# Kernel tuning notes

Measured on AMD Instinct MI355X. Metric: run time of the kernel, lower is better.

The kernel has to match this reference:

```python
import jax, jax.numpy as jnp
import numpy as np

RES_SAMPLE = [-0.4, -0.3, -0.2, -0.1, 0.0, 0.1, 0.2, 0.3, 0.4]
GROUP_NUM = 8


def setup_inputs() -> dict:
    key = jax.random.key(0)
    k1, k2, k3, k4 = jax.random.split(key, 4)
    B, C, H, W = 4, 32, 256, 256
    return {
        "feat_ref": jax.random.normal(k1, (B, C, H, W), dtype=jnp.float32),
        "feat_ls": jax.random.normal(k2, (B, C, H, W), dtype=jnp.float32),
        "feat_rs": jax.random.normal(k3, (B, C, H, W), dtype=jnp.float32),
        "disp_init": jax.random.uniform(k4, (B, 1, H, W), dtype=jnp.float32),
    }


def _bilerp_chw(feat, x, y):
    """Bilinear sample feat [C,H,W] at pixel coords x,y [H,W], zeros padding
    (matches F.grid_sample(mode='bilinear', padding_mode='zeros'))."""
    C, H, W = feat.shape
    x0 = jnp.floor(x); y0 = jnp.floor(y)
    x1 = x0 + 1.0;     y1 = y0 + 1.0
    wx1 = x - x0; wx0 = 1.0 - wx1
    wy1 = y - y0; wy0 = 1.0 - wy1

    def gather(yi, xi):
        valid = (yi >= 0) & (yi <= H - 1) & (xi >= 0) & (xi <= W - 1)
        yc = jnp.clip(yi, 0, H - 1).astype(jnp.int32)
        xc = jnp.clip(xi, 0, W - 1).astype(jnp.int32)
        return feat[:, yc, xc] * valid.astype(feat.dtype)  # [C,H,W]

    return (gather(y0, x0) * (wy0 * wx0)
            + gather(y0, x1) * (wy0 * wx1)
            + gather(y1, x0) * (wy1 * wx0)
            + gather(y1, x1) * (wy1 * wx1))


def _warp_all_disp(feat, disp, x_dist):
    """feat [B,C,H,W], disp [B,D,H,W] -> warped [B,C,D,H,W] (y_dist=0)."""
    B, C, H, W = feat.shape
    xx = jnp.arange(W, dtype=feat.dtype)[None, :] * jnp.ones((H, 1), feat.dtype)  # [H,W]
    yy = jnp.arange(H, dtype=feat.dtype)[:, None] * jnp.ones((1, W), feat.dtype)  # [H,W]

    def per_b(feat_b, disp_b):  # feat_b [C,H,W], disp_b [D,H,W]
        x = xx[None] + x_dist * disp_b                      # [D,H,W]
        y = jnp.broadcast_to(yy, x.shape)                   # [D,H,W]
        return jax.vmap(lambda xs, ys: _bilerp_chw(feat_b, xs, ys))(x, y)  # [D,C,H,W]

    out = jax.vmap(per_b)(feat, disp)                       # [B,D,C,H,W]
    return out.transpose(0, 2, 1, 3, 4)                     # [B,C,D,H,W]


def reference(feat_ref, feat_ls, feat_rs, disp_init):
    B, C, H, W = feat_ref.shape
    res = jnp.asarray(RES_SAMPLE, dtype=feat_ref.dtype)     # [D]
    D = res.shape[0]
    disp = disp_init[:, 0][:, None] + res[None, :, None, None]  # [B,D,H,W]

    warp_left = _warp_all_disp(feat_ls, disp, 1.0)          # [B,C,D,H,W]
    warp_right = _warp_all_disp(feat_rs, disp, -1.0)        # [B,C,D,H,W]
    fr = feat_ref[:, :, None]                                # [B,C,1,H,W]

    mu = (warp_left + warp_right + fr) / 3.0
    var = ((warp_left - mu) ** 2 + (warp_right - mu) ** 2 + (fr - mu) ** 2) / 3.0

    cpg = C // GROUP_NUM
    cost = var.reshape(B, GROUP_NUM, cpg, D, H, W).mean(axis=2)  # [B,G,D,H,W]
    return cost
```

## Files before the change

### kernel.cpp

```cpp
#include <hip/hip_runtime.h>


#define B_ 4
#define C_ 32
#define H_ 256
#define W_ 256
#define D_ 9
#define G_ 8
#define CPG 4
#define HW_ (H_ * W_)

typedef float v2f __attribute__((ext_vector_type(2)));

__global__ __launch_bounds__(256) void cost_volume_kernel(
    const float* __restrict__ fref,
    const float* __restrict__ fls,
    const float* __restrict__ frs,
    const float* __restrict__ disp0,
    float* __restrict__ out)
{
    const float res[D_] = {-0.4f, -0.3f, -0.2f, -0.1f, 0.0f,
                            0.1f,  0.2f,  0.3f,  0.4f};
    int g2 = blockIdx.x & 3;
    int t  = blockIdx.x >> 2;
    int h  = t & (H_ - 1);
    int b  = t >> 8;
    int w  = threadIdx.x;

    float dbase = disp0[((size_t)b * H_ + h) * W_ + w];

    int i0l = (int)floorf((float)w + (dbase + res[0]));
    int i0r = (int)floorf((float)w - (dbase + res[8]));

    float vl[3], vr[3];
    int il[3], ir[3];
    #pragma unroll
    for (int k = 0; k < 3; ++k) {
        int a = i0l + k;
        vl[k] = (a >= 0 && a < W_) ? 1.0f : 0.0f;
        il[k] = min(max(a, 0), W_ - 1);
        int c = i0r + k;
        vr[k] = (c >= 0 && c < W_) ? 1.0f : 0.0f;
        ir[k] = min(max(c, 0), W_ - 1);
    }

    float la[D_], lb[D_], lc[D_];
    float ra[D_], rb[D_], rc[D_];
    #pragma unroll
    for (int d = 0; d < D_; ++d) {
        float disp = dbase + res[d];

        float xl = (float)w + disp;
        float fl = floorf(xl);
        float w1 = xl - fl;
        float w0 = 1.0f - w1;
        bool jl = ((int)fl != i0l);
        la[d] = jl ? 0.0f : w0 * vl[0];
        lb[d] = jl ? w0 * vl[1] : w1 * vl[1];
        lc[d] = jl ? w1 * vl[2] : 0.0f;

        float xr = (float)w - disp;
        float fx = floorf(xr);
        float u1 = xr - fx;
        float u0 = 1.0f - u1;
        bool jr = ((int)fx != i0r);
        ra[d] = jr ? 0.0f : u0 * vr[0];
        rb[d] = jr ? u0 * vr[1] : u1 * vr[1];
        rc[d] = jr ? u1 * vr[2] : 0.0f;
    }

    size_t base = (size_t)b * C_ * HW_ + (size_t)h * W_;
    const float* pref = fref + base;
    const float* pls  = fls  + base;
    const float* prs  = frs  + base;

    size_t obase = (size_t)b * G_ * D_ * HW_ + (size_t)h * W_ + w;

    #pragma unroll 1
    for (int gi = 0; gi < 2; ++gi) {
        int g = g2 * 2 + gi;
        v2f acc[D_];
        #pragma unroll
        for (int d = 0; d < D_; ++d) acc[d] = (v2f)(0.0f);

        #pragma unroll
        for (int p = 0; p < 2; ++p) {
            size_t c0 = (size_t)(g * CPG + p * 2) * HW_;
            const float* rrow = pref + c0;
            const float* lrow = pls + c0;
            const float* rsw  = prs + c0;

            v2f fr = { rrow[w],      rrow[HW_ + w] };
            v2f t0 = { lrow[il[0]],  lrow[HW_ + il[0]] };
            v2f t1 = { lrow[il[1]],  lrow[HW_ + il[1]] };
            v2f t2 = { lrow[il[2]],  lrow[HW_ + il[2]] };
            v2f u0 = { rsw[ir[0]],   rsw[HW_ + ir[0]] };
            v2f u1 = { rsw[ir[1]],   rsw[HW_ + ir[1]] };
            v2f u2 = { rsw[ir[2]],   rsw[HW_ + ir[2]] };

            v2f fr2 = fr * fr;

            #pragma unroll
            for (int d = 0; d < D_; ++d) {
                v2f wl = t0 * la[d] + t1 * lb[d] + t2 * lc[d];
                v2f wr = u0 * ra[d] + u1 * rb[d] + u2 * rc[d];
                v2f s  = wl + wr + fr;
                v2f q  = __builtin_elementwise_fma(
                             wl, wl, __builtin_elementwise_fma(wr, wr, fr2));
                acc[d] += q - s * s * (1.0f / 3.0f);
            }
        }

        #pragma unroll
        for (int d = 0; d < D_; ++d) {
            float v = (acc[d].x + acc[d].y) * (1.0f / 12.0f);
            out[obase + (size_t)(g * D_ + d) * HW_] = v;
        }
    }
}

extern "C" void kernel_launch(void* const* d_in, const int* in_sizes, int n_in,
                              void* d_out, int out_size, void* d_ws, size_t ws_size,
                              hipStream_t stream) {
    const float* fref  = (const float*)d_in[0];
    const float* fls   = (const float*)d_in[1];
    const float* frs   = (const float*)d_in[2];
    const float* disp0 = (const float*)d_in[3];
    float* out = (float*)d_out;

    dim3 grid(B_ * H_ * 4);
    dim3 block(W_);
    cost_volume_kernel<<<grid, block, 0, stream>>>(fref, fls, frs, disp0, out);
}
```

Measured before the change: 170.0 us.

## Stage warped feature rows in LDS via async global_load_lds with zero padding

```diff
diff --git a/kernel.cpp b/kernel.cpp
--- a/kernel.cpp
+++ b/kernel.cpp
@@ -7,12 +7,12 @@
 #define W_ 256
 #define D_ 9
 #define G_ 8
-#define CPG 4
 #define HW_ (H_ * W_)
+#define RSTRIDE 264
 
 typedef float v2f __attribute__((ext_vector_type(2)));
 
-__global__ __launch_bounds__(256) void cost_volume_kernel(
+__global__ __launch_bounds__(256, 4) void cost_volume_kernel(
     const float* __restrict__ fref,
     const float* __restrict__ fls,
     const float* __restrict__ frs,
@@ -21,28 +21,42 @@
 {
     const float res[D_] = {-0.4f, -0.3f, -0.2f, -0.1f, 0.0f,
                             0.1f,  0.2f,  0.3f,  0.4f};
+    __shared__ float smem[16 * RSTRIDE];
+
     int g2 = blockIdx.x & 3;
     int t  = blockIdx.x >> 2;
     int h  = t & (H_ - 1);
     int b  = t >> 8;
     int w  = threadIdx.x;
+    int lane = w & 63;
+    int wave = w >> 6;
+
+    size_t base = (size_t)b * C_ * HW_ + (size_t)h * W_ + (size_t)(g2 * 8) * HW_;
+    const float* pref = fref + base;
+    const float* pls  = fls  + base;
+    const float* prs  = frs  + base;
+
+    #pragma unroll
+    for (int rr = 0; rr < 4; ++rr) {
+        int r  = wave * 4 + rr;
+        int ch = r & 7;
+        const float* grow = ((r < 8) ? pls : prs) + (size_t)ch * HW_ + lane * 4;
+        float* lrow = smem + r * RSTRIDE + 4 + lane * 4;
+        __builtin_amdgcn_global_load_lds(
+            (__attribute__((address_space(1))) unsigned int*)(unsigned long long)grow,
+            (__attribute__((address_space(3))) unsigned int*)lrow,
+            16, 0, 0);
+    }
+    if (w < 128) {
+        int r = w >> 3;
+        int k = w & 7;
+        smem[r * RSTRIDE + ((k < 4) ? k : (256 + k))] = 0.0f;
+    }
 
     float dbase = disp0[((size_t)b * H_ + h) * W_ + w];
 
     int i0l = (int)floorf((float)w + (dbase + res[0]));
     int i0r = (int)floorf((float)w - (dbase + res[8]));
-
-    float vl[3], vr[3];
-    int il[3], ir[3];
-    #pragma unroll
-    for (int k = 0; k < 3; ++k) {
-        int a = i0l + k;
-        vl[k] = (a >= 0 && a < W_) ? 1.0f : 0.0f;
-        il[k] = min(max(a, 0), W_ - 1);
-        int c = i0r + k;
-        vr[k] = (c >= 0 && c < W_) ? 1.0f : 0.0f;
-        ir[k] = min(max(c, 0), W_ - 1);
-    }
 
     float la[D_], lb[D_], lc[D_];
     float ra[D_], rb[D_], rc[D_];
@@ -52,51 +66,55 @@
 
         float xl = (float)w + disp;
         float fl = floorf(xl);
-        float w1 = xl - fl;
-        float w0 = 1.0f - w1;
+        float f1 = xl - fl;
+        float f0 = 1.0f - f1;
         bool jl = ((int)fl != i0l);
-        la[d] = jl ? 0.0f : w0 * vl[0];
-        lb[d] = jl ? w0 * vl[1] : w1 * vl[1];
-        lc[d] = jl ? w1 * vl[2] : 0.0f;
+        la[d] = jl ? 0.0f : f0;
+        lb[d] = jl ? f0 : f1;
+        lc[d] = jl ? f1 : 0.0f;
 
         float xr = (float)w - disp;
         float fx = floorf(xr);
         float u1 = xr - fx;
         float u0 = 1.0f - u1;
         bool jr = ((int)fx != i0r);
-        ra[d] = jr ? 0.0f : u0 * vr[0];
-        rb[d] = jr ? u0 * vr[1] : u1 * vr[1];
-        rc[d] = jr ? u1 * vr[2] : 0.0f;
+        ra[d] = jr ? 0.0f : u0;
+        rb[d] = jr ? u0 : u1;
+        rc[d] = jr ? u1 : 0.0f;
     }
 
-    size_t base = (size_t)b * C_ * HW_ + (size_t)h * W_;
-    const float* pref = fref + base;
-    const float* pls  = fls  + base;
-    const float* prs  = frs  + base;
+    __syncthreads();
 
-    size_t obase = (size_t)b * G_ * D_ * HW_ + (size_t)h * W_ + w;
+    int idxL = 4 + i0l;
+    int idxR = 4 + i0r;
+
+    size_t obase = ((size_t)b * G_ + g2 * 2) * D_ * HW_ + (size_t)h * W_ + w;
 
     #pragma unroll 1
-    for (int gi = 0; gi < 2; ++gi) {
-        int g = g2 * 2 + gi;
+    for (int gc = 0; gc < 2; ++gc) {
         v2f acc[D_];
         #pragma unroll
         for (int d = 0; d < D_; ++d) acc[d] = (v2f)(0.0f);
 
         #pragma unroll
         for (int p = 0; p < 2; ++p) {
-            size_t c0 = (size_t)(g * CPG + p * 2) * HW_;
-            const float* rrow = pref + c0;
-            const float* lrow = pls + c0;
-            const float* rsw  = prs + c0;
+            int c0 = gc * 4 + p * 2;
 
-            v2f fr = { rrow[w],      rrow[HW_ + w] };
-            v2f t0 = { lrow[il[0]],  lrow[HW_ + il[0]] };
-            v2f t1 = { lrow[il[1]],  lrow[HW_ + il[1]] };
-            v2f t2 = { lrow[il[2]],  lrow[HW_ + il[2]] };
-            v2f u0 = { rsw[ir[0]],   rsw[HW_ + ir[0]] };
-            v2f u1 = { rsw[ir[1]],   rsw[HW_ + ir[1]] };
-            v2f u2 = { rsw[ir[2]],   rsw[HW_ + ir[2]] };
+            v2f fr = { pref[(size_t)c0 * HW_ + w],
+                       pref[(size_t)(c0 + 1) * HW_ + w] };
+
+            v2f t0 = { smem[ c0      * RSTRIDE + idxL    ],
+                       smem[(c0 + 1) * RSTRIDE + idxL    ] };
+            v2f t1 = { smem[ c0      * RSTRIDE + idxL + 1],
+                       smem[(c0 + 1) * RSTRIDE + idxL + 1] };
+            v2f t2 = { smem[ c0      * RSTRIDE + idxL + 2],
+                       smem[(c0 + 1) * RSTRIDE + idxL + 2] };
+            v2f u0 = { smem[(8 + c0    ) * RSTRIDE + idxR    ],
+                       smem[(8 + c0 + 1) * RSTRIDE + idxR    ] };
+            v2f u1 = { smem[(8 + c0    ) * RSTRIDE + idxR + 1],
+                       smem[(8 + c0 + 1) * RSTRIDE + idxR + 1] };
+            v2f u2 = { smem[(8 + c0    ) * RSTRIDE + idxR + 2],
+                       smem[(8 + c0 + 1) * RSTRIDE + idxR + 2] };
 
             v2f fr2 = fr * fr;
 
@@ -107,14 +125,15 @@
                 v2f s  = wl + wr + fr;
                 v2f q  = __builtin_elementwise_fma(
                              wl, wl, __builtin_elementwise_fma(wr, wr, fr2));
-                acc[d] += q - s * s * (1.0f / 3.0f);
+                acc[d] = __builtin_elementwise_fma(
+                             s * s, (v2f)(-1.0f / 3.0f), acc[d] + q);
             }
         }
 
         #pragma unroll
         for (int d = 0; d < D_; ++d) {
-            float v = (acc[d].x + acc[d].y) * (1.0f / 12.0f);
-            out[obase + (size_t)(g * D_ + d) * HW_] = v;
+            out[obase + (size_t)(gc * D_ + d) * HW_] =
+                (acc[d].x + acc[d].y) * (1.0f / 12.0f);
         }
     }
 }
```

Measured after the change: 375.2 us. 2.21x slower.
